# Kernel optimization log

Hardware: AMD Instinct MI355X
Metric: run time of the kernel (lower is better)

Reference implementation:

```python
import jax, jax.numpy as jnp
import numpy as np
import math

THETA = 10000.0
NUM_HEADS = 16


def _rope(x, pos, theta):
    # x: [B, H, S, d_k], pos: [S] int
    d_k = x.shape[-1]
    inv_freq = 1.0 / (theta ** (jnp.arange(0, d_k, 2, dtype=jnp.float32) / d_k))  # [d_k/2]
    freqs = pos.astype(jnp.float32)[:, None] * inv_freq[None, :]  # [S, d_k/2]
    cos = jnp.cos(freqs)  # broadcast over B, H
    sin = jnp.sin(freqs)
    x_even = x[..., 0::2]
    x_odd = x[..., 1::2]
    r_even = x_even * cos - x_odd * sin
    r_odd = x_even * sin + x_odd * cos
    # interleave back: [..., S, d_k/2, 2] -> [..., S, d_k]
    return jnp.stack([r_even, r_odd], axis=-1).reshape(x.shape)


def setup_inputs() -> dict:
    key = jax.random.key(0)
    ks = jax.random.split(key, 5)
    B, S, D = 2, 2048, 1024
    sigma = math.sqrt(2.0 / (D + D))
    return {
        "x": jax.random.normal(ks[0], (B, S, D), dtype=jnp.float32),
        "Wq": jax.random.normal(ks[1], (D, D), dtype=jnp.float32) * sigma,
        "Wk": jax.random.normal(ks[2], (D, D), dtype=jnp.float32) * sigma,
        "Wv": jax.random.normal(ks[3], (D, D), dtype=jnp.float32) * sigma,
        "Wo": jax.random.normal(ks[4], (D, D), dtype=jnp.float32) * sigma,
        "token_positions": jnp.arange(S, dtype=jnp.int32),
    }


def reference(x, Wq, Wk, Wv, Wo, token_positions):
    B, S, D = x.shape
    H = NUM_HEADS
    d_k = D // H

    def split_heads(t):  # [B,S,D] -> [B,H,S,d_k]
        return t.reshape(B, S, H, d_k).transpose(0, 2, 1, 3)

    q = split_heads(x @ Wq.T)
    k = split_heads(x @ Wk.T)
    v = split_heads(x @ Wv.T)

    q = _rope(q, token_positions, THETA)
    k = _rope(k, token_positions, THETA)

    scores = jnp.einsum("bhqd,bhkd->bhqk", q, k) / jnp.sqrt(jnp.float32(d_k))
    causal = jnp.tril(jnp.ones((S, S), dtype=bool))
    scores = jnp.where(causal, scores, jnp.finfo(scores.dtype).min)
    probs = jax.nn.softmax(scores, axis=-1)
    attn = jnp.einsum("bhqk,bhkd->bhqd", probs, v)  # [B,H,S,d_k]

    attn = attn.transpose(0, 2, 1, 3).reshape(B, S, D)
    return attn @ Wo.T
```

## Files before the change

### kernel.cpp

```cpp
#include <hip/hip_runtime.h>
#include <hip/hip_bf16.h>

#define B_ 2
#define S_ 2048
#define D_ 1024
#define H_ 16
#define DK_ 64
#define M_ (B_*S_)
#define K_ D_

typedef __attribute__((ext_vector_type(8))) short bf16x8;
typedef __attribute__((ext_vector_type(4))) float f32x4;

__device__ __forceinline__ unsigned short f2bf(float f) {
  unsigned u = __float_as_uint(f);
  u += 0x7fff + ((u >> 16) & 1);
  return (unsigned short)(u >> 16);
}

__device__ __forceinline__ void gload_lds16(const void* g, void* l) {
  __builtin_amdgcn_global_load_lds(
      (const __attribute__((address_space(1))) unsigned int*)(unsigned long long)g,
      (__attribute__((address_space(3))) unsigned int*)(unsigned int)(unsigned long long)l,
      16, 0, 0);
}

__global__ __launch_bounds__(256) void k_cvt(
    const float* __restrict__ x,
    const float* __restrict__ w0, const float* __restrict__ w1,
    const float* __restrict__ w2, const float* __restrict__ w3,
    unsigned short* __restrict__ xb, unsigned short* __restrict__ wb,
    const int* __restrict__ pos, float2* __restrict__ tab) {
  const int bid = blockIdx.x;
  if (bid >= 8192) {
    int t = (bid - 8192) * 256 + threadIdx.x;
    int s = t >> 5, j = t & 31;
    float inv = powf(10000.0f, -(float)j / 32.0f);
    float ang = (float)pos[s] * inv;
    tab[t] = make_float2(cosf(ang), sinf(ang));
    return;
  }
  const float* sp;
  unsigned short* dp;
  size_t off;
  if (bid < 4096) {
    sp = x; dp = xb; off = (size_t)bid * 1024 + threadIdx.x * 4;
  } else {
    const int wi = (bid - 4096) >> 10;
    sp = (wi == 0) ? w0 : (wi == 1) ? w1 : (wi == 2) ? w2 : w3;
    dp = wb + (size_t)wi * D_ * K_;
    off = (size_t)((bid - 4096) & 1023) * 1024 + threadIdx.x * 4;
  }
  float4 v = *(const float4*)(sp + off);
  ushort4 o;
  o.x = f2bf(v.x); o.y = f2bf(v.y); o.z = f2bf(v.z); o.w = f2bf(v.w);
  *(ushort4*)(dp + off) = o;
}

__global__ __launch_bounds__(512, 4) void k_gemm0(
    const unsigned short* __restrict__ A,
    const unsigned short* __restrict__ Wall,
    unsigned short* __restrict__ qkv,
    const float2* __restrict__ tab)
{
  __shared__ unsigned short SA[2][128*64];
  __shared__ unsigned short SB[2][192*64];
  const int tid = threadIdx.x, lane = tid & 63, w = tid >> 6;
  const int wr = w >> 2, wc = w & 3;
  const int c = lane & 15, hg = lane >> 4;
  const int m0 = blockIdx.x * 128;
  const int n0 = blockIdx.y * 192;
  const unsigned short* Ag = A + (size_t)m0 * K_;
  const unsigned short* Bg = Wall + (size_t)n0 * K_;

  f32x4 acc[4][3];
#pragma unroll
  for (int m = 0; m < 4; ++m)
#pragma unroll
    for (int n = 0; n < 3; ++n) acc[m][n] = (f32x4){0.f, 0.f, 0.f, 0.f};

  const int srow   = w*8 + (lane >> 3);
  const int schunk = (lane & 7) ^ (lane >> 3);

#define GS0(KT, BI)                                                           \
  do {                                                                        \
    _Pragma("unroll")                                                         \
    for (int i = 0; i < 2; ++i)                                               \
      gload_lds16(Ag + (size_t)(i*64 + srow)*K_ + (KT) + schunk*8,            \
                  &SA[BI][(i*64 + w*8)*64]);                                  \
    _Pragma("unroll")                                                         \
    for (int i = 0; i < 3; ++i)                                               \
      gload_lds16(Bg + (size_t)(i*64 + srow)*K_ + (KT) + schunk*8,            \
                  &SB[BI][(i*64 + w*8)*64]);                                  \
  } while (0)

  GS0(0, 0);
  for (int t = 0; t < K_/64; ++t) {
    asm volatile("s_waitcnt vmcnt(0)" ::: "memory");
    __builtin_amdgcn_s_barrier();
    asm volatile("" ::: "memory");
    if (t + 1 < K_/64) GS0((t+1)*64, (t & 1) ^ 1);

    const int bi = t & 1;
#pragma unroll
    for (int kk = 0; kk < 2; ++kk) {
      bf16x8 af[4], bfr[3];
#pragma unroll
      for (int m = 0; m < 4; ++m)
        af[m] = *(const bf16x8*)&SA[bi][(wr*64 + m*16 + c)*64 + (((kk*4 + hg) ^ (c & 7))*8)];
#pragma unroll
      for (int n = 0; n < 3; ++n)
        bfr[n] = *(const bf16x8*)&SB[bi][(wc*48 + n*16 + c)*64 + (((kk*4 + hg) ^ (c & 7))*8)];
#pragma unroll
      for (int m = 0; m < 4; ++m)
#pragma unroll
        for (int n = 0; n < 3; ++n)
          acc[m][n] = __builtin_amdgcn_mfma_f32_16x16x32_bf16(af[m], bfr[n], acc[m][n], 0, 0, 0);
    }
  }
#undef GS0

#pragma unroll
  for (int m = 0; m < 4; ++m)
#pragma unroll
    for (int n = 0; n < 3; ++n) {
      const int row0 = m0 + wr*64 + m*16 + hg*4;
      const int col  = n0 + wc*48 + n*16 + c;
      const int z = col >> 10;
      const int colz = col & 1023;
      const int h = colz >> 6, d = colz & 63;
      unsigned short* dst = qkv + (size_t)z * M_ * D_;
      if (z == 2) {
        const int b = row0 >> 11, s0 = row0 & (S_ - 1);
        ushort4 o;
        o.x = f2bf(acc[m][n][0]); o.y = f2bf(acc[m][n][1]);
        o.z = f2bf(acc[m][n][2]); o.w = f2bf(acc[m][n][3]);
        *(ushort4*)&dst[((size_t)(b*H_ + h)*DK_ + d)*S_ + s0] = o;
      } else {
        const float post = (z == 0) ? 0.18033688f : 1.0f;
        const float sgn = (d & 1) ? 1.0f : -1.0f;
#pragma unroll
        for (int r = 0; r < 4; ++r) {
          const int row = row0 + r;
          const int b = row >> 11, s = row & (S_ - 1);
          float v  = acc[m][n][r];
          float pv = __shfl_xor(v, 1);
          float2 cs = tab[s*32 + (d >> 1)];
          float ov = (v * cs.x + sgn * pv * cs.y) * post;
          dst[((size_t)(b*H_ + h)*S_ + s)*DK_ + d] = f2bf(ov);
        }
      }
    }
}

__global__ __launch_bounds__(512, 4) void k_gemm1(
    const unsigned short* __restrict__ A,
    const unsigned short* __restrict__ Wo,
    float* __restrict__ fout)
{
  __shared__ unsigned short As[2][64*64];
  __shared__ unsigned short Bs[2][128*64];
  const int tid = threadIdx.x, lane = tid & 63, w = tid >> 6;
  const int wr = w >> 2, wc = w & 3;
  const int c = lane & 15, hg = lane >> 4;
  const int m0 = blockIdx.x * 64, n0 = blockIdx.y * 128;
  const unsigned short* Ag = A + (size_t)m0 * K_;
  const unsigned short* Bg = Wo + (size_t)n0 * K_;

  f32x4 acc[2][2];
#pragma unroll
  for (int m = 0; m < 2; ++m)
#pragma unroll
    for (int n = 0; n < 2; ++n) acc[m][n] = (f32x4){0.f, 0.f, 0.f, 0.f};

  const int srow   = w*8 + (lane >> 3);
  const int schunk = (lane & 7) ^ (lane >> 3);

#define GS1(KT, BI)                                                           \
  do {                                                                        \
    gload_lds16(Ag + (size_t)srow*K_ + (KT) + schunk*8,                       \
                &As[BI][(w*8)*64]);                                           \
    _Pragma("unroll")                                                         \
    for (int i = 0; i < 2; ++i)                                               \
      gload_lds16(Bg + (size_t)(i*64 + srow)*K_ + (KT) + schunk*8,            \
                  &Bs[BI][(i*64 + w*8)*64]);                                  \
  } while (0)

  GS1(0, 0);
  for (int t = 0; t < K_/64; ++t) {
    asm volatile("s_waitcnt vmcnt(0)" ::: "memory");
    __builtin_amdgcn_s_barrier();
    asm volatile("" ::: "memory");
    if (t + 1 < K_/64) GS1((t+1)*64, (t & 1) ^ 1);

    const int bi = t & 1;
#pragma unroll
    for (int kk = 0; kk < 2; ++kk) {
      bf16x8 af[2], bfr[2];
#pragma unroll
      for (int m = 0; m < 2; ++m)
        af[m] = *(const bf16x8*)&As[bi][(wr*32 + m*16 + c)*64 + (((kk*4 + hg) ^ (c & 7))*8)];
#pragma unroll
      for (int n = 0; n < 2; ++n)
        bfr[n] = *(const bf16x8*)&Bs[bi][(wc*32 + n*16 + c)*64 + (((kk*4 + hg) ^ (c & 7))*8)];
#pragma unroll
      for (int m = 0; m < 2; ++m)
#pragma unroll
        for (int n = 0; n < 2; ++n)
          acc[m][n] = __builtin_amdgcn_mfma_f32_16x16x32_bf16(af[m], bfr[n], acc[m][n], 0, 0, 0);
    }
  }
#undef GS1

#pragma unroll
  for (int m = 0; m < 2; ++m)
#pragma unroll
    for (int n = 0; n < 2; ++n) {
      const int row0 = m0 + wr*32 + m*16 + hg*4;
      const int col  = n0 + wc*32 + n*16 + c;
#pragma unroll
      for (int r = 0; r < 4; ++r)
        fout[(size_t)(row0 + r)*D_ + col] = acc[m][n][r];
    }
}

__global__ __launch_bounds__(256) void k_attn(
    const unsigned short* __restrict__ Qg,
    const unsigned short* __restrict__ Kg,
    const unsigned short* __restrict__ Vtg,
    unsigned short* __restrict__ Og)
{
  __shared__ unsigned short Kb[3][64*64];
  __shared__ unsigned short Vb[3][64*64];
  __shared__ unsigned short Ps[4][32*72];

  const int tid = threadIdx.x, lane = tid & 63, w = tid >> 6;
  const int bid = blockIdx.x;
  const int xcd = bid & 7, idx = bid >> 3;
  const int head = xcd * 4 + (idx & 3);
  const int p  = (idx < 32) ? (idx >> 2) : (15 - ((idx - 32) >> 2));
  const int hv = 31 - p;
  const int c = lane & 15, hg = lane >> 4;
  const int q0m[2] = { hv*64 + w*16, p*64 + w*16 };

  const unsigned short* Qp = Qg + (size_t)head * S_ * DK_;
  const unsigned short* Kp = Kg + (size_t)head * S_ * DK_;
  const unsigned short* Vp = Vtg + (size_t)head * DK_ * S_;

  const int srow   = w*8 + (lane >> 3);
  const int schunk = (lane & 7) ^ (lane >> 3);

  const short ONE_BF = (short)0x3F80;
  const bf16x8 vones = {ONE_BF, ONE_BF, ONE_BF, ONE_BF, ONE_BF, ONE_BF, ONE_BF, ONE_BF};
  const f32x4 NEG8 = {-8.f, -8.f, -8.f, -8.f};

  bf16x8 aq[2][2];
#pragma unroll
  for (int m = 0; m < 2; ++m)
#pragma unroll
    for (int kk = 0; kk < 2; ++kk)
      aq[m][kk] = *(const bf16x8*)(Qp + (size_t)(q0m[m] + c)*DK_ + kk*32 + hg*8);

  f32x4 oacc[2][4], lacc[2];
#pragma unroll
  for (int m = 0; m < 2; ++m) {
#pragma unroll
    for (int n = 0; n < 4; ++n) oacc[m][n] = (f32x4){0.f, 0.f, 0.f, 0.f};
    lacc[m] = (f32x4){0.f, 0.f, 0.f, 0.f};
  }

  const int nkv = hv + 1;

#define STAGE(T, BI)                                                          \
  do {                                                                        \
    const int kv0s = (T) * 64;                                                \
    _Pragma("unroll")                                                         \
    for (int i = 0; i < 2; ++i) {                                             \
      gload_lds16(Kp + (size_t)(kv0s + i*32 + srow)*DK_ + schunk*8,           \
                  &Kb[BI][(i*32 + w*8)*64]);                                  \
      gload_lds16(Vp + (size_t)(i*32 + srow)*S_ + kv0s + schunk*8,            \
                  &Vb[BI][(i*32 + w*8)*64]);                                  \
    }                                                                         \
  } while (0)

  STAGE(0, 0);
  if (nkv > 1) STAGE(1, 1);

  int cb = 0;
  for (int t = 0; t < nkv; ++t) {
    if (t + 1 < nkv) { asm volatile("s_waitcnt vmcnt(4)" ::: "memory"); }
    else             { asm volatile("s_waitcnt vmcnt(0)" ::: "memory"); }
    __builtin_amdgcn_s_barrier();
    asm volatile("" ::: "memory");
    if (t + 2 < nkv) {
      int sb = cb + 2; if (sb >= 3) sb -= 3;
      STAGE(t + 2, sb);
    }

    const int kv0 = t * 64;
    const bool live1 = (t <= p);

    bf16x8 bk[4][2];
#pragma unroll
    for (int n = 0; n < 4; ++n)
#pragma unroll
      for (int kk = 0; kk < 2; ++kk)
        bk[n][kk] = *(const bf16x8*)&Kb[cb][(n*16 + c)*64 + (((kk*4 + hg) ^ (c & 7))*8)];

    f32x4 sc4[2][4];
    __builtin_amdgcn_s_setprio(1);
#pragma unroll
    for (int m = 0; m < 2; ++m) {
      if (m == 1 && !live1) break;
#pragma unroll
      for (int n = 0; n < 4; ++n) {
        sc4[m][n] = __builtin_amdgcn_mfma_f32_16x16x32_bf16(bk[n][0], aq[m][0], NEG8, 0, 0, 0);
        sc4[m][n] = __builtin_amdgcn_mfma_f32_16x16x32_bf16(bk[n][1], aq[m][1], sc4[m][n], 0, 0, 0);
      }
    }
    __builtin_amdgcn_s_setprio(0);

    bf16x8 bv[4][2];
#pragma unroll
    for (int n = 0; n < 4; ++n)
#pragma unroll
      for (int kk = 0; kk < 2; ++kk)
        bv[n][kk] = *(const bf16x8*)&Vb[cb][(n*16 + c)*64 + (((kk*4 + hg) ^ (c & 7))*8)];

#pragma unroll
    for (int m = 0; m < 2; ++m) {
      if (m == 1 && !live1) continue;
      const int tm = (m == 0) ? hv : p;
      const int qg = q0m[m] + c;
      if (t == tm) {
#pragma unroll
        for (int n = 0; n < 4; ++n)
#pragma unroll
          for (int r = 0; r < 4; ++r)
            if (kv0 + n*16 + hg*4 + r > qg) sc4[m][n][r] = -INFINITY;
      }

#pragma unroll
      for (int n = 0; n < 4; ++n) {
        union { __hip_bfloat162 h2[2]; ushort4 u; } pk;
        pk.h2[0] = __float22bfloat162_rn(make_float2(
            __builtin_amdgcn_exp2f(sc4[m][n][0]),
            __builtin_amdgcn_exp2f(sc4[m][n][1])));
        pk.h2[1] = __float22bfloat162_rn(make_float2(
            __builtin_amdgcn_exp2f(sc4[m][n][2]),
            __builtin_amdgcn_exp2f(sc4[m][n][3])));
        *(ushort4*)&Ps[w][(m*16 + c)*72 + n*16 + hg*4] = pk.u;
      }

      bf16x8 ap[2];
#pragma unroll
      for (int kk = 0; kk < 2; ++kk)
        ap[kk] = *(const bf16x8*)&Ps[w][(m*16 + c)*72 + kk*32 + hg*8];
      __builtin_amdgcn_s_setprio(1);
#pragma unroll
      for (int n = 0; n < 4; ++n)
#pragma unroll
        for (int kk = 0; kk < 2; ++kk)
          oacc[m][n] = __builtin_amdgcn_mfma_f32_16x16x32_bf16(ap[kk], bv[n][kk], oacc[m][n], 0, 0, 0);
#pragma unroll
      for (int kk = 0; kk < 2; ++kk)
        lacc[m] = __builtin_amdgcn_mfma_f32_16x16x32_bf16(ap[kk], vones, lacc[m], 0, 0, 0);
      __builtin_amdgcn_s_setprio(0);
    }

    asm volatile("" ::: "memory");
    if (++cb == 3) cb = 0;
  }
#undef STAGE

  const int b = head >> 4, h = head & 15;
#pragma unroll
  for (int m = 0; m < 2; ++m) {
    float rl[4];
#pragma unroll
    for (int r = 0; r < 4; ++r) rl[r] = 1.0f / lacc[m][r];
#pragma unroll
    for (int n = 0; n < 4; ++n)
#pragma unroll
      for (int r = 0; r < 4; ++r) {
        const int s = q0m[m] + hg*4 + r;
        const int d = n*16 + c;
        Og[((size_t)b*S_ + s)*D_ + h*DK_ + d] = f2bf(oacc[m][n][r] * rl[r]);
      }
  }
}

extern "C" void kernel_launch(void* const* d_in, const int* in_sizes, int n_in,
                              void* d_out, int out_size, void* d_ws, size_t ws_size,
                              hipStream_t stream) {
  const float* x = (const float*)d_in[0];
  const float* Wm[4] = {(const float*)d_in[1], (const float*)d_in[2],
                        (const float*)d_in[3], (const float*)d_in[4]};
  const int* tp = (const int*)d_in[5];
  float* out = (float*)d_out;

  unsigned short* ws = (unsigned short*)d_ws;
  const size_t MD = (size_t)M_ * D_;
  unsigned short* xb  = ws;
  unsigned short* wb  = ws + MD;
  unsigned short* qws = ws + MD + 4*(size_t)D_*K_;
  float2* tab = (float2*)(ws + MD + 4*(size_t)D_*K_ + 3*MD);

  k_cvt<<<dim3(8448), 256, 0, stream>>>(x, Wm[0], Wm[1], Wm[2], Wm[3], xb, wb, tp, tab);

  k_gemm0<<<dim3(M_/128, 16), 512, 0, stream>>>(xb, wb, qws, tab);

  unsigned short* attn = xb;
  k_attn<<<dim3(512), 256, 0, stream>>>(qws, qws + MD, qws + 2*MD, attn);

  k_gemm1<<<dim3(M_/64, D_/128), 512, 0, stream>>>(attn, wb + 3*(size_t)D_*K_, out);
}
```

Before: 90.77 us.

## Split paired-query attention blocks into one q-tile per block, double-buffer

The attention kernel drops the scheme where each block handled two paired query tiles (a high one and its mirror low one) for causal load balancing. Each block now handles one 64-row query tile, and the grid doubles to 1024 blocks scheduled heaviest-first. The K/V prefetch goes from a 3-stage ring to a 2-stage double buffer with a full vmcnt(0) wait every iteration. This cuts LDS and register use and raises block count, at the cost of reloading K/V per block, less latency hiding, and uneven per-block work.

```diff
diff --git a/kernel.cpp b/kernel.cpp
--- a/kernel.cpp
+++ b/kernel.cpp
@@ -230,18 +230,17 @@
     const unsigned short* __restrict__ Vtg,
     unsigned short* __restrict__ Og)
 {
-  __shared__ unsigned short Kb[3][64*64];
-  __shared__ unsigned short Vb[3][64*64];
-  __shared__ unsigned short Ps[4][32*72];
+  __shared__ unsigned short Kb[2][64*64];
+  __shared__ unsigned short Vb[2][64*64];
+  __shared__ unsigned short Ps[4][16*72];
 
   const int tid = threadIdx.x, lane = tid & 63, w = tid >> 6;
   const int bid = blockIdx.x;
-  const int xcd = bid & 7, idx = bid >> 3;
-  const int head = xcd * 4 + (idx & 3);
-  const int p  = (idx < 32) ? (idx >> 2) : (15 - ((idx - 32) >> 2));
-  const int hv = 31 - p;
+  const int xcd = bid & 7, sub = (bid >> 3) & 3;
+  const int head = xcd * 4 + sub;
+  const int qt = 31 - (bid >> 5);
+  const int q0 = qt * 64 + w * 16;
   const int c = lane & 15, hg = lane >> 4;
-  const int q0m[2] = { hv*64 + w*16, p*64 + w*16 };
 
   const unsigned short* Qp = Qg + (size_t)head * S_ * DK_;
   const unsigned short* Kp = Kg + (size_t)head * S_ * DK_;
@@ -254,22 +253,17 @@
   const bf16x8 vones = {ONE_BF, ONE_BF, ONE_BF, ONE_BF, ONE_BF, ONE_BF, ONE_BF, ONE_BF};
   const f32x4 NEG8 = {-8.f, -8.f, -8.f, -8.f};
 
-  bf16x8 aq[2][2];
-#pragma unroll
-  for (int m = 0; m < 2; ++m)
-#pragma unroll
-    for (int kk = 0; kk < 2; ++kk)
-      aq[m][kk] = *(const bf16x8*)(Qp + (size_t)(q0m[m] + c)*DK_ + kk*32 + hg*8);
-
-  f32x4 oacc[2][4], lacc[2];
-#pragma unroll
-  for (int m = 0; m < 2; ++m) {
-#pragma unroll
-    for (int n = 0; n < 4; ++n) oacc[m][n] = (f32x4){0.f, 0.f, 0.f, 0.f};
-    lacc[m] = (f32x4){0.f, 0.f, 0.f, 0.f};
-  }
-
-  const int nkv = hv + 1;
+  bf16x8 aq[2];
+#pragma unroll
+  for (int kk = 0; kk < 2; ++kk)
+    aq[kk] = *(const bf16x8*)(Qp + (size_t)(q0 + c)*DK_ + kk*32 + hg*8);
+
+  f32x4 oacc[4], lacc;
+#pragma unroll
+  for (int n = 0; n < 4; ++n) oacc[n] = (f32x4){0.f, 0.f, 0.f, 0.f};
+  lacc = (f32x4){0.f, 0.f, 0.f, 0.f};
+
+  const int nkv = qt + 1;
 
 #define STAGE(T, BI)                                                          \
   do {                                                                        \
@@ -284,39 +278,29 @@
   } while (0)
 
   STAGE(0, 0);
-  if (nkv > 1) STAGE(1, 1);
-
-  int cb = 0;
+
   for (int t = 0; t < nkv; ++t) {
-    if (t + 1 < nkv) { asm volatile("s_waitcnt vmcnt(4)" ::: "memory"); }
-    else             { asm volatile("s_waitcnt vmcnt(0)" ::: "memory"); }
+    const int bi = t & 1;
+    asm volatile("s_waitcnt vmcnt(0)" ::: "memory");
     __builtin_amdgcn_s_barrier();
     asm volatile("" ::: "memory");
-    if (t + 2 < nkv) {
-      int sb = cb + 2; if (sb >= 3) sb -= 3;
-      STAGE(t + 2, sb);
-    }
+    if (t + 1 < nkv) STAGE(t + 1, bi ^ 1);
 
     const int kv0 = t * 64;
-    const bool live1 = (t <= p);
 
     bf16x8 bk[4][2];
 #pragma unroll
     for (int n = 0; n < 4; ++n)
 #pragma unroll
       for (int kk = 0; kk < 2; ++kk)
-        bk[n][kk] = *(const bf16x8*)&Kb[cb][(n*16 + c)*64 + (((kk*4 + hg) ^ (c & 7))*8)];
-
-    f32x4 sc4[2][4];
+        bk[n][kk] = *(const bf16x8*)&Kb[bi][(n*16 + c)*64 + (((kk*4 + hg) ^ (c & 7))*8)];
+
+    f32x4 sc4[4];
     __builtin_amdgcn_s_setprio(1);
 #pragma unroll
-    for (int m = 0; m < 2; ++m) {
-      if (m == 1 && !live1) break;
-#pragma unroll
-      for (int n = 0; n < 4; ++n) {
-        sc4[m][n] = __builtin_amdgcn_mfma_f32_16x16x32_bf16(bk[n][0], aq[m][0], NEG8, 0, 0, 0);
-        sc4[m][n] = __builtin_amdgcn_mfma_f32_16x16x32_bf16(bk[n][1], aq[m][1], sc4[m][n], 0, 0, 0);
-      }
+    for (int n = 0; n < 4; ++n) {
+      sc4[n] = __builtin_amdgcn_mfma_f32_16x16x32_bf16(bk[n][0], aq[0], NEG8, 0, 0, 0);
+      sc4[n] = __builtin_amdgcn_mfma_f32_16x16x32_bf16(bk[n][1], aq[1], sc4[n], 0, 0, 0);
     }
     __builtin_amdgcn_s_setprio(0);
 
@@ -325,69 +309,60 @@
     for (int n = 0; n < 4; ++n)
 #pragma unroll
       for (int kk = 0; kk < 2; ++kk)
-        bv[n][kk] = *(const bf16x8*)&Vb[cb][(n*16 + c)*64 + (((kk*4 + hg) ^ (c & 7))*8)];
-
-#pragma unroll
-    for (int m = 0; m < 2; ++m) {
-      if (m == 1 && !live1) continue;
-      const int tm = (m == 0) ? hv : p;
-      const int qg = q0m[m] + c;
-      if (t == tm) {
-#pragma unroll
-        for (int n = 0; n < 4; ++n)
-#pragma unroll
-          for (int r = 0; r < 4; ++r)
-            if (kv0 + n*16 + hg*4 + r > qg) sc4[m][n][r] = -INFINITY;
-      }
-
-#pragma unroll
-      for (int n = 0; n < 4; ++n) {
-        union { __hip_bfloat162 h2[2]; ushort4 u; } pk;
-        pk.h2[0] = __float22bfloat162_rn(make_float2(
-            __builtin_amdgcn_exp2f(sc4[m][n][0]),
-            __builtin_amdgcn_exp2f(sc4[m][n][1])));
-        pk.h2[1] = __float22bfloat162_rn(make_float2(
-            __builtin_amdgcn_exp2f(sc4[m][n][2]),
-            __builtin_amdgcn_exp2f(sc4[m][n][3])));
-        *(ushort4*)&Ps[w][(m*16 + c)*72 + n*16 + hg*4] = pk.u;
-      }
-
-      bf16x8 ap[2];
+        bv[n][kk] = *(const bf16x8*)&Vb[bi][(n*16 + c)*64 + (((kk*4 + hg) ^ (c & 7))*8)];
+
+    if (t == qt) {
+      const int qg = q0 + c;
+#pragma unroll
+      for (int n = 0; n < 4; ++n)
+#pragma unroll
+        for (int r = 0; r < 4; ++r)
+          if (kv0 + n*16 + hg*4 + r > qg) sc4[n][r] = -INFINITY;
+    }
+
+#pragma unroll
+    for (int n = 0; n < 4; ++n) {
+      union { __hip_bfloat162 h2[2]; ushort4 u; } pk;
+      pk.h2[0] = __float22bfloat162_rn(make_float2(
+          __builtin_amdgcn_exp2f(sc4[n][0]),
+          __builtin_amdgcn_exp2f(sc4[n][1])));
+      pk.h2[1] = __float22bfloat162_rn(make_float2(
+          __builtin_amdgcn_exp2f(sc4[n][2]),
+          __builtin_amdgcn_exp2f(sc4[n][3])));
+      *(ushort4*)&Ps[w][c*72 + n*16 + hg*4] = pk.u;
+    }
+
+    bf16x8 ap[2];
+#pragma unroll
+    for (int kk = 0; kk < 2; ++kk)
+      ap[kk] = *(const bf16x8*)&Ps[w][c*72 + kk*32 + hg*8];
+    __builtin_amdgcn_s_setprio(1);
+#pragma unroll
+    for (int n = 0; n < 4; ++n)
 #pragma unroll
       for (int kk = 0; kk < 2; ++kk)
-        ap[kk] = *(const bf16x8*)&Ps[w][(m*16 + c)*72 + kk*32 + hg*8];
-      __builtin_amdgcn_s_setprio(1);
-#pragma unroll
-      for (int n = 0; n < 4; ++n)
-#pragma unroll
-        for (int kk = 0; kk < 2; ++kk)
-          oacc[m][n] = __builtin_amdgcn_mfma_f32_16x16x32_bf16(ap[kk], bv[n][kk], oacc[m][n], 0, 0, 0);
-#pragma unroll
-      for (int kk = 0; kk < 2; ++kk)
-        lacc[m] = __builtin_amdgcn_mfma_f32_16x16x32_bf16(ap[kk], vones, lacc[m], 0, 0, 0);
-      __builtin_amdgcn_s_setprio(0);
-    }
+        oacc[n] = __builtin_amdgcn_mfma_f32_16x16x32_bf16(ap[kk], bv[n][kk], oacc[n], 0, 0, 0);
+#pragma unroll
+    for (int kk = 0; kk < 2; ++kk)
+      lacc = __builtin_amdgcn_mfma_f32_16x16x32_bf16(ap[kk], vones, lacc, 0, 0, 0);
+    __builtin_amdgcn_s_setprio(0);
 
     asm volatile("" ::: "memory");
-    if (++cb == 3) cb = 0;
   }
 #undef STAGE
 
   const int b = head >> 4, h = head & 15;
-#pragma unroll
-  for (int m = 0; m < 2; ++m) {
-    float rl[4];
-#pragma unroll
-    for (int r = 0; r < 4; ++r) rl[r] = 1.0f / lacc[m][r];
-#pragma unroll
-    for (int n = 0; n < 4; ++n)
-#pragma unroll
-      for (int r = 0; r < 4; ++r) {
-        const int s = q0m[m] + hg*4 + r;
-        const int d = n*16 + c;
-        Og[((size_t)b*S_ + s)*D_ + h*DK_ + d] = f2bf(oacc[m][n][r] * rl[r]);
-      }
-  }
+  float rl[4];
+#pragma unroll
+  for (int r = 0; r < 4; ++r) rl[r] = 1.0f / lacc[r];
+#pragma unroll
+  for (int n = 0; n < 4; ++n)
+#pragma unroll
+    for (int r = 0; r < 4; ++r) {
+      const int s = q0 + hg*4 + r;
+      const int d = n*16 + c;
+      Og[((size_t)b*S_ + s)*D_ + h*DK_ + d] = f2bf(oacc[n][r] * rl[r]);
+    }
 }
 
 extern "C" void kernel_launch(void* const* d_in, const int* in_sizes, int n_in,
@@ -411,7 +386,7 @@
   k_gemm0<<<dim3(M_/128, 16), 512, 0, stream>>>(xb, wb, qws, tab);
 
   unsigned short* attn = xb;
-  k_attn<<<dim3(512), 256, 0, stream>>>(qws, qws + MD, qws + 2*MD, attn);
+  k_attn<<<dim3(1024), 256, 0, stream>>>(qws, qws + MD, qws + 2*MD, attn);
 
   k_gemm1<<<dim3(M_/64, D_/128), 512, 0, stream>>>(attn, wb + 3*(size_t)D_*K_, out);
 }
```

Measured after the change: 87.22 us, median of 4. 1.04x faster.

## Split attention into one 64-query tile per block with 2-wave blocks, double buffering

Applied to the files above, without the earlier changes.

Replaces the paired causal query tiles per block (a heavy and a light tile sharing one KV stream) with one 64-row query tile per 128-thread block, giving 1024 blocks scheduled heaviest-first. KV staging drops from triple to double buffering, with a full vmcnt(0) wait each iteration. This makes blocks smaller and more numerous, aiming for better occupancy and load balance. In exchange, K/V tiles are no longer shared between two query tiles, and the shallower prefetch exposes more memory latency.

```diff
diff --git a/kernel.cpp b/kernel.cpp
--- a/kernel.cpp
+++ b/kernel.cpp
@@ -224,24 +224,23 @@
     }
 }
 
-__global__ __launch_bounds__(256) void k_attn(
+__global__ __launch_bounds__(128) void k_attn(
     const unsigned short* __restrict__ Qg,
     const unsigned short* __restrict__ Kg,
     const unsigned short* __restrict__ Vtg,
     unsigned short* __restrict__ Og)
 {
-  __shared__ unsigned short Kb[3][64*64];
-  __shared__ unsigned short Vb[3][64*64];
-  __shared__ unsigned short Ps[4][32*72];
+  __shared__ unsigned short Kb[2][64*64];
+  __shared__ unsigned short Vb[2][64*64];
+  __shared__ unsigned short Ps[2][32*72];
 
   const int tid = threadIdx.x, lane = tid & 63, w = tid >> 6;
   const int bid = blockIdx.x;
-  const int xcd = bid & 7, idx = bid >> 3;
-  const int head = xcd * 4 + (idx & 3);
-  const int p  = (idx < 32) ? (idx >> 2) : (15 - ((idx - 32) >> 2));
-  const int hv = 31 - p;
+  const int xcd = bid & 7, sub = (bid >> 3) & 3;
+  const int head = xcd * 4 + sub;
+  const int qt = 31 - (bid >> 5);
   const int c = lane & 15, hg = lane >> 4;
-  const int q0m[2] = { hv*64 + w*16, p*64 + w*16 };
+  const int q0m[2] = { qt*64 + w*32, qt*64 + w*32 + 16 };
 
   const unsigned short* Qp = Qg + (size_t)head * S_ * DK_;
   const unsigned short* Kp = Kg + (size_t)head * S_ * DK_;
@@ -269,55 +268,47 @@
     lacc[m] = (f32x4){0.f, 0.f, 0.f, 0.f};
   }
 
-  const int nkv = hv + 1;
+  const int nkv = qt + 1;
 
 #define STAGE(T, BI)                                                          \
   do {                                                                        \
     const int kv0s = (T) * 64;                                                \
     _Pragma("unroll")                                                         \
-    for (int i = 0; i < 2; ++i) {                                             \
-      gload_lds16(Kp + (size_t)(kv0s + i*32 + srow)*DK_ + schunk*8,           \
-                  &Kb[BI][(i*32 + w*8)*64]);                                  \
-      gload_lds16(Vp + (size_t)(i*32 + srow)*S_ + kv0s + schunk*8,            \
-                  &Vb[BI][(i*32 + w*8)*64]);                                  \
+    for (int i = 0; i < 4; ++i) {                                             \
+      gload_lds16(Kp + (size_t)(kv0s + i*16 + srow)*DK_ + schunk*8,           \
+                  &Kb[BI][(i*16 + w*8)*64]);                                  \
+      gload_lds16(Vp + (size_t)(i*16 + srow)*S_ + kv0s + schunk*8,            \
+                  &Vb[BI][(i*16 + w*8)*64]);                                  \
     }                                                                         \
   } while (0)
 
   STAGE(0, 0);
-  if (nkv > 1) STAGE(1, 1);
-
-  int cb = 0;
+
   for (int t = 0; t < nkv; ++t) {
-    if (t + 1 < nkv) { asm volatile("s_waitcnt vmcnt(4)" ::: "memory"); }
-    else             { asm volatile("s_waitcnt vmcnt(0)" ::: "memory"); }
+    const int bi = t & 1;
+    asm volatile("s_waitcnt vmcnt(0)" ::: "memory");
     __builtin_amdgcn_s_barrier();
     asm volatile("" ::: "memory");
-    if (t + 2 < nkv) {
-      int sb = cb + 2; if (sb >= 3) sb -= 3;
-      STAGE(t + 2, sb);
-    }
+    if (t + 1 < nkv) STAGE(t + 1, bi ^ 1);
 
     const int kv0 = t * 64;
-    const bool live1 = (t <= p);
 
     bf16x8 bk[4][2];
 #pragma unroll
     for (int n = 0; n < 4; ++n)
 #pragma unroll
       for (int kk = 0; kk < 2; ++kk)
-        bk[n][kk] = *(const bf16x8*)&Kb[cb][(n*16 + c)*64 + (((kk*4 + hg) ^ (c & 7))*8)];
+        bk[n][kk] = *(const bf16x8*)&Kb[bi][(n*16 + c)*64 + (((kk*4 + hg) ^ (c & 7))*8)];
 
     f32x4 sc4[2][4];
     __builtin_amdgcn_s_setprio(1);
 #pragma unroll
-    for (int m = 0; m < 2; ++m) {
-      if (m == 1 && !live1) break;
+    for (int m = 0; m < 2; ++m)
 #pragma unroll
       for (int n = 0; n < 4; ++n) {
         sc4[m][n] = __builtin_amdgcn_mfma_f32_16x16x32_bf16(bk[n][0], aq[m][0], NEG8, 0, 0, 0);
         sc4[m][n] = __builtin_amdgcn_mfma_f32_16x16x32_bf16(bk[n][1], aq[m][1], sc4[m][n], 0, 0, 0);
       }
-    }
     __builtin_amdgcn_s_setprio(0);
 
     bf16x8 bv[4][2];
@@ -325,14 +316,14 @@
     for (int n = 0; n < 4; ++n)
 #pragma unroll
       for (int kk = 0; kk < 2; ++kk)
-        bv[n][kk] = *(const bf16x8*)&Vb[cb][(n*16 + c)*64 + (((kk*4 + hg) ^ (c & 7))*8)];
+        bv[n][kk] = *(const bf16x8*)&Vb[bi][(n*16 + c)*64 + (((kk*4 + hg) ^ (c & 7))*8)];
+
+    const bool diag = (t == qt);
 
 #pragma unroll
     for (int m = 0; m < 2; ++m) {
-      if (m == 1 && !live1) continue;
-      const int tm = (m == 0) ? hv : p;
-      const int qg = q0m[m] + c;
-      if (t == tm) {
+      if (diag) {
+        const int qg = q0m[m] + c;
 #pragma unroll
         for (int n = 0; n < 4; ++n)
 #pragma unroll
@@ -369,7 +360,6 @@
     }
 
     asm volatile("" ::: "memory");
-    if (++cb == 3) cb = 0;
   }
 #undef STAGE
 
@@ -411,7 +401,7 @@
   k_gemm0<<<dim3(M_/128, 16), 512, 0, stream>>>(xb, wb, qws, tab);
 
   unsigned short* attn = xb;
-  k_attn<<<dim3(512), 256, 0, stream>>>(qws, qws + MD, qws + 2*MD, attn);
+  k_attn<<<dim3(1024), 128, 0, stream>>>(qws, qws + MD, qws + 2*MD, attn);
 
   k_gemm1<<<dim3(M_/64, D_/128), 512, 0, stream>>>(attn, wb + 3*(size_t)D_*K_, out);
 }
```

Result: slower. 96.88 us (+6.7%).
